# Optimization experiments

Hardware: AMD Instinct MI355X
Metric: run time of the kernel (lower is better)

The kernel has to match this reference:

```python
import jax, jax.numpy as jnp
import numpy as np

B, H, T, OUT, MLP_H = 4096, 1024, 60, 2, 64
IN = H + 4

def setup_inputs() -> dict:
    key = jax.random.key(0)
    ks = jax.random.split(key, 12)
    s = 1.0 / np.sqrt(H)
    return {
        "z": jax.random.normal(ks[0], (B, H), jnp.float32),
        "last_vel": jax.random.normal(ks[1], (B, 2), jnp.float32),
        "last_pos": jax.random.normal(ks[2], (B, 2), jnp.float32),
        "W_ih": jax.random.uniform(ks[3], (4 * H, IN), jnp.float32, -s, s),
        "W_hh": jax.random.uniform(ks[4], (4 * H, H), jnp.float32, -s, s),
        "b_ih": jax.random.uniform(ks[5], (4 * H,), jnp.float32, -s, s),
        "b_hh": jax.random.uniform(ks[6], (4 * H,), jnp.float32, -s, s),
        "W1": jax.random.uniform(ks[7], (MLP_H, H), jnp.float32, -s, s),
        "b1": jax.random.uniform(ks[8], (MLP_H,), jnp.float32, -s, s),
        "W2": jax.random.uniform(ks[9], (OUT, MLP_H), jnp.float32, -s, s),
        "b2": jax.random.uniform(ks[10], (OUT,), jnp.float32, -s, s),
    }

def _forward(z, last_vel, last_pos, W_ih, W_hh, b_ih, b_hh, W1, b1, W2, b2):
    z_aug = jnp.concatenate([z, last_pos, last_vel], axis=-1)  # (B, H+4)
    # input is identical at every timestep -> precompute input projection once
    x_gates = z_aug @ W_ih.T + b_ih + b_hh  # (B, 4H)

    def step(carry, _):
        h, c = carry
        gates = x_gates + h @ W_hh.T  # (B, 4H)
        i, f, g, o = jnp.split(gates, 4, axis=-1)  # torch gate order i,f,g,o
        i = jax.nn.sigmoid(i)
        f = jax.nn.sigmoid(f)
        g = jnp.tanh(g)
        o = jax.nn.sigmoid(o)
        c = f * c + i * g
        h = o * jnp.tanh(c)
        return (h, c), h

    h0 = jnp.zeros((z.shape[0], W_hh.shape[1]), z.dtype)
    _, hs = jax.lax.scan(step, (h0, h0), None, length=T)  # (T, B, H)
    out = jnp.transpose(hs, (1, 0, 2))  # (B, T, H)
    delta = jax.nn.relu(out @ W1.T + b1) @ W2.T + b2  # (B, T, 2)
    return jnp.cumsum(delta, axis=1) + last_pos[:, None, :]

def reference(z, last_vel, last_pos, W_ih, W_hh, b_ih, b_hh, W1, b1, W2, b2):
    return _forward(z, last_vel, last_pos, W_ih, W_hh, b_ih, b_hh, W1, b1, W2, b2)
```

## Files before the change

kernel.cpp:

```cpp
#include <hip/hip_runtime.h>
#include <stdint.h>

#define B_    4096
#define H_    1024
#define T_    60
#define IN_   1028
#define KA_   1056
#define G4_   4096
#define MLPH_ 64
#define NB_   6

typedef __attribute__((ext_vector_type(8))) short bf16x8;
typedef __attribute__((ext_vector_type(4))) float f32x4;
typedef __attribute__((ext_vector_type(4))) unsigned short u16x4;

#define GLOBAL_AS __attribute__((address_space(1)))
#define LDS_AS    __attribute__((address_space(3)))

__device__ __forceinline__ void gload_lds16(const void* g, void* l) {
  __builtin_amdgcn_global_load_lds((GLOBAL_AS void*)const_cast<void*>(g),
                                   (LDS_AS void*)l, 16, 0, 0);
}

__device__ __forceinline__ unsigned short f2bf(float f) {
  union { float f; unsigned int u; } v; v.f = f;
  unsigned int r = v.u + 0x7FFFu + ((v.u >> 16) & 1u);
  return (unsigned short)(r >> 16);
}

__device__ __forceinline__ float bf2f(unsigned short u) {
  union { unsigned int u; float f; } v; v.u = ((unsigned int)u) << 16;
  return v.f;
}

__device__ __forceinline__ float sigmf(float x) {
  float e = __expf(-x);
  return __builtin_amdgcn_rcpf(1.0f + e);
}

__device__ __forceinline__ float tanh_fast(float x) {
  x = fminf(fmaxf(x, -15.0f), 15.0f);
  float e = __expf(2.0f * x);
  return (e - 1.0f) * __builtin_amdgcn_rcpf(e + 1.0f);
}


__global__ void k_conv_bf16(const float* __restrict__ src,
                            unsigned short* __restrict__ dst, int n) {
  int i = blockIdx.x * blockDim.x + threadIdx.x;
  int stride = gridDim.x * blockDim.x;
  for (; i < n; i += stride) dst[i] = f2bf(src[i]);
}

__global__ void k_conv_wih(const float* __restrict__ w,
                           unsigned short* __restrict__ dst) {
  int i = blockIdx.x * blockDim.x + threadIdx.x;
  int stride = gridDim.x * blockDim.x;
  const int n = G4_ * KA_;
  for (; i < n; i += stride) {
    int r = i / KA_, k = i - r * KA_;
    dst[i] = (k < IN_) ? f2bf(w[(size_t)r * IN_ + k]) : (unsigned short)0;
  }
}

__global__ void k_build_zaug(const float* __restrict__ z,
                             const float* __restrict__ lp,
                             const float* __restrict__ lv,
                             unsigned short* __restrict__ dst) {
  int i = blockIdx.x * blockDim.x + threadIdx.x;
  int stride = gridDim.x * blockDim.x;
  const int n = B_ * KA_;
  for (; i < n; i += stride) {
    int b = i / KA_, k = i - b * KA_;
    float v;
    if (k < H_)            v = z[(size_t)b * H_ + k];
    else if (k < H_ + 2)   v = lp[b * 2 + (k - H_)];
    else if (k < IN_)      v = lv[b * 2 + (k - H_ - 2)];
    else                   v = 0.0f;
    dst[i] = f2bf(v);
  }
}


__global__ __launch_bounds__(256, 3) void k_xgates(
    const unsigned short* __restrict__ zaug, const unsigned short* __restrict__ wih,
    const float* __restrict__ bih, const float* __restrict__ bhh,
    u16x4* __restrict__ xg4) {
  __shared__ unsigned short As[128 * 32];
  __shared__ unsigned short Bs[128 * 32];
  const int tid = threadIdx.x, lane = tid & 63, wave = tid >> 6;
  const int bx = blockIdx.x, by = blockIdx.y;
  const int r_sub = lane >> 2;
  const int c16 = (lane & 3) * 16;

  f32x4 acc[2][8];
#pragma unroll
  for (int m = 0; m < 2; ++m)
#pragma unroll
    for (int n = 0; n < 8; ++n) acc[m][n] = {0.f, 0.f, 0.f, 0.f};

  for (int kk = 0; kk < KA_ / 32; ++kk) {
    const int k0 = kk * 32;
    __syncthreads();
#pragma unroll
    for (int i = 0; i < 2; ++i) {
      int ch = wave * 2 + i;
      int row = bx * 128 + ch * 16 + r_sub;
      gload_lds16((const char*)zaug + ((size_t)row * KA_ + k0) * 2 + c16,
                  (char*)As + ch * 1024);
    }
#pragma unroll
    for (int i = 0; i < 2; ++i) {
      int ch = wave * 2 + i;
      int g = ch >> 1;
      int wrow = g * H_ + by * 32 + (ch & 1) * 16 + r_sub;
      gload_lds16((const char*)wih + ((size_t)wrow * KA_ + k0) * 2 + c16,
                  (char*)Bs + ch * 1024);
    }
    __syncthreads();
    bf16x8 a[2], b[8];
#pragma unroll
    for (int m = 0; m < 2; ++m)
      a[m] = *(const bf16x8*)&As[(wave * 32 + m * 16 + (lane & 15)) * 32 + (lane >> 4) * 8];
#pragma unroll
    for (int n = 0; n < 8; ++n)
      b[n] = *(const bf16x8*)&Bs[(n * 16 + (lane & 15)) * 32 + (lane >> 4) * 8];
#pragma unroll
    for (int m = 0; m < 2; ++m)
#pragma unroll
      for (int n = 0; n < 8; ++n)
        acc[m][n] = __builtin_amdgcn_mfma_f32_16x16x32_bf16(a[m], b[n], acc[m][n], 0, 0, 0);
  }

  const int r0 = (lane >> 4) * 4, cl = lane & 15;
#pragma unroll
  for (int m = 0; m < 2; ++m)
#pragma unroll
    for (int j = 0; j < 4; ++j) {
      int row = bx * 128 + wave * 32 + m * 16 + r0 + j;
#pragma unroll
      for (int p = 0; p < 2; ++p) {
        int hc = by * 32 + p * 16 + cl;
        float iv = acc[m][0 + p][j] + bih[hc]        + bhh[hc];
        float fv = acc[m][2 + p][j] + bih[1024 + hc] + bhh[1024 + hc];
        float gv = acc[m][4 + p][j] + bih[2048 + hc] + bhh[2048 + hc];
        float ov = acc[m][6 + p][j] + bih[3072 + hc] + bhh[3072 + hc];
        u16x4 st = {f2bf(iv), f2bf(fv), f2bf(gv), f2bf(ov)};
        xg4[(size_t)row * H_ + hc] = st;
      }
    }
}


__global__ __launch_bounds__(256, 3) void k_step(
    const unsigned short* __restrict__ hprev, const unsigned short* __restrict__ whh,
    const u16x4* __restrict__ xg4, float* __restrict__ cbuf,
    unsigned short* __restrict__ hout) {
  __shared__ unsigned short As[128 * 32];
  __shared__ unsigned short Bs[128 * 32];
  const int tid = threadIdx.x, lane = tid & 63, wave = tid >> 6;
  const int bx = blockIdx.x, by = blockIdx.y;
  const int r_sub = lane >> 2;
  const int c16 = (lane & 3) * 16;

  f32x4 acc[2][8];
#pragma unroll
  for (int m = 0; m < 2; ++m)
#pragma unroll
    for (int n = 0; n < 8; ++n) acc[m][n] = {0.f, 0.f, 0.f, 0.f};

  for (int kk = 0; kk < H_ / 32; ++kk) {
    const int k0 = kk * 32;
    __syncthreads();
#pragma unroll
    for (int i = 0; i < 2; ++i) {
      int ch = wave * 2 + i;
      int row = bx * 128 + ch * 16 + r_sub;
      gload_lds16((const char*)hprev + ((size_t)row * H_ + k0) * 2 + c16,
                  (char*)As + ch * 1024);
    }
#pragma unroll
    for (int i = 0; i < 2; ++i) {
      int ch = wave * 2 + i;
      int g = ch >> 1;
      int wrow = g * H_ + by * 32 + (ch & 1) * 16 + r_sub;
      gload_lds16((const char*)whh + ((size_t)wrow * H_ + k0) * 2 + c16,
                  (char*)Bs + ch * 1024);
    }
    __syncthreads();
    bf16x8 a[2], b[8];
#pragma unroll
    for (int m = 0; m < 2; ++m)
      a[m] = *(const bf16x8*)&As[(wave * 32 + m * 16 + (lane & 15)) * 32 + (lane >> 4) * 8];
#pragma unroll
    for (int n = 0; n < 8; ++n)
      b[n] = *(const bf16x8*)&Bs[(n * 16 + (lane & 15)) * 32 + (lane >> 4) * 8];
#pragma unroll
    for (int m = 0; m < 2; ++m)
#pragma unroll
      for (int n = 0; n < 8; ++n)
        acc[m][n] = __builtin_amdgcn_mfma_f32_16x16x32_bf16(a[m], b[n], acc[m][n], 0, 0, 0);
  }

  const int r0 = (lane >> 4) * 4, cl = lane & 15;
#pragma unroll
  for (int m = 0; m < 2; ++m)
#pragma unroll
    for (int j = 0; j < 4; ++j) {
      int row = bx * 128 + wave * 32 + m * 16 + r0 + j;
#pragma unroll
      for (int p = 0; p < 2; ++p) {
        int hc = by * 32 + p * 16 + cl;
        u16x4 xv = xg4[(size_t)row * H_ + hc];
        float iv = sigmf(acc[m][0 + p][j] + bf2f(xv[0]));
        float fv = sigmf(acc[m][2 + p][j] + bf2f(xv[1]));
        float gv = tanh_fast(acc[m][4 + p][j] + bf2f(xv[2]));
        float ov = sigmf(acc[m][6 + p][j] + bf2f(xv[3]));
        size_t ci = (size_t)row * H_ + hc;
        float cv = fv * cbuf[ci] + iv * gv;
        cbuf[ci] = cv;
        hout[ci] = f2bf(ov * tanh_fast(cv));
      }
    }
}


__global__ __launch_bounds__(256) void k_mlp(
    const unsigned short* __restrict__ hring, const unsigned short* __restrict__ w1,
    const float* __restrict__ b1, const float* __restrict__ w2,
    const float* __restrict__ b2, float* __restrict__ delta, int t0) {
  __shared__ unsigned short As[64 * 32];
  __shared__ unsigned short Bs[64 * 32];
  __shared__ float hid[64][65];
  const int tid = threadIdx.x, lane = tid & 63, wave = tid >> 6;
  const int bx = blockIdx.x;
  const unsigned short* h = hring + (size_t)blockIdx.y * B_ * H_;
  const int t = t0 + blockIdx.y;
  const int r_sub = lane >> 2;
  const int c16 = (lane & 3) * 16;

  f32x4 acc[4];
#pragma unroll
  for (int n = 0; n < 4; ++n) acc[n] = {0.f, 0.f, 0.f, 0.f};

  for (int kk = 0; kk < H_ / 32; ++kk) {
    const int k0 = kk * 32;
    __syncthreads();
    {
      int row = bx * 64 + wave * 16 + r_sub;
      gload_lds16((const char*)h + ((size_t)row * H_ + k0) * 2 + c16,
                  (char*)As + wave * 1024);
    }
    {
      int jj = wave * 16 + r_sub;
      gload_lds16((const char*)w1 + ((size_t)jj * H_ + k0) * 2 + c16,
                  (char*)Bs + wave * 1024);
    }
    __syncthreads();
    bf16x8 a = *(const bf16x8*)&As[(wave * 16 + (lane & 15)) * 32 + (lane >> 4) * 8];
#pragma unroll
    for (int n = 0; n < 4; ++n) {
      bf16x8 b = *(const bf16x8*)&Bs[(n * 16 + (lane & 15)) * 32 + (lane >> 4) * 8];
      acc[n] = __builtin_amdgcn_mfma_f32_16x16x32_bf16(a, b, acc[n], 0, 0, 0);
    }
  }

  const int r0 = (lane >> 4) * 4, cl = lane & 15;
#pragma unroll
  for (int n = 0; n < 4; ++n)
#pragma unroll
    for (int j = 0; j < 4; ++j) {
      int row = wave * 16 + r0 + j;
      int col = n * 16 + cl;
      hid[row][col] = fmaxf(acc[n][j] + b1[col], 0.0f);
    }
  __syncthreads();

  if (tid < 128) {
    int r = tid >> 1, d = tid & 1;
    float s = b2[d];
#pragma unroll 8
    for (int k2 = 0; k2 < 64; ++k2) s += hid[r][k2] * w2[d * 64 + k2];
    delta[((size_t)(bx * 64 + r) * T_ + t) * 2 + d] = s;
  }
}


__global__ void k_cumsum(const float* __restrict__ delta,
                         const float* __restrict__ lp, float* __restrict__ out) {
  int id = blockIdx.x * blockDim.x + threadIdx.x;
  if (id >= B_ * 2) return;
  int b = id >> 1, d = id & 1;
  float cum = lp[b * 2 + d];
  size_t base = (size_t)b * T_ * 2 + d;
  for (int t = 0; t < T_; ++t) {
    cum += delta[base + t * 2];
    out[base + t * 2] = cum;
  }
}


extern "C" void kernel_launch(void* const* d_in, const int* in_sizes, int n_in,
                              void* d_out, int out_size, void* d_ws, size_t ws_size,
                              hipStream_t stream) {
  const float* z   = (const float*)d_in[0];
  const float* lv  = (const float*)d_in[1];
  const float* lp  = (const float*)d_in[2];
  const float* Wih = (const float*)d_in[3];
  const float* Whh = (const float*)d_in[4];
  const float* bih = (const float*)d_in[5];
  const float* bhh = (const float*)d_in[6];
  const float* W1  = (const float*)d_in[7];
  const float* b1  = (const float*)d_in[8];
  const float* W2  = (const float*)d_in[9];
  const float* b2  = (const float*)d_in[10];
  float* out = (float*)d_out;

  char* ws = (char*)d_ws;
  size_t off = 0;
  u16x4*          xg4    = (u16x4*)(ws + off);          off += (size_t)B_ * H_ * 8;
  unsigned short* whh_bf = (unsigned short*)(ws + off); off += (size_t)G4_ * H_ * 2;
  unsigned short* wih_bf = (unsigned short*)(ws + off); off += (size_t)G4_ * KA_ * 2;
  unsigned short* zaug   = (unsigned short*)(ws + off); off += (size_t)B_ * KA_ * 2;
  unsigned short* w1_bf  = (unsigned short*)(ws + off); off += (size_t)MLPH_ * H_ * 2;
  unsigned short* hring  = (unsigned short*)(ws + off); off += (size_t)NB_ * B_ * H_ * 2;
  float*          cbuf   = (float*)(ws + off);          off += (size_t)B_ * H_ * 4;
  float*          delta  = (float*)(ws + off);          off += (size_t)B_ * T_ * 2 * 4;

  const size_t BH = (size_t)B_ * H_;

  hipMemsetAsync(hring + (NB_ - 1) * BH, 0, BH * 2, stream);
  hipMemsetAsync(cbuf, 0, BH * 4, stream);

  k_conv_bf16 <<<2048, 256, 0, stream>>>(Whh, whh_bf, G4_ * H_);
  k_conv_wih  <<<2048, 256, 0, stream>>>(Wih, wih_bf);
  k_build_zaug<<<2048, 256, 0, stream>>>(z, lp, lv, zaug);
  k_conv_bf16 <<<256, 256, 0, stream>>>(W1, w1_bf, MLPH_ * H_);

  k_xgates<<<dim3(32, 32), 256, 0, stream>>>(zaug, wih_bf, bih, bhh, xg4);

  for (int t = 0; t < T_; ++t) {
    const unsigned short* hp = hring + (size_t)((t + NB_ - 1) % NB_) * BH;
    unsigned short*       hc = hring + (size_t)(t % NB_) * BH;
    k_step<<<dim3(32, 32), 256, 0, stream>>>(hp, whh_bf, xg4, cbuf, hc);
    if ((t % NB_) == NB_ - 1)
      k_mlp<<<dim3(64, NB_), 256, 0, stream>>>(hring, w1_bf, b1, W2, b2, delta, t - (NB_ - 1));
  }

  k_cumsum<<<32, 256, 0, stream>>>(delta, lp, out);
}
```

Before: 3.540 ms.

## Double-buffer LDS tiles and use 2x2 wave layout in LSTM GEMM kernels

Both the input-projection and recurrent-step GEMM kernels now double-buffer their LDS tiles. The next K-slice is prefetched with global_load_lds while MFMAs run on the current one, which removes one barrier per iteration. Waves are rearranged into a 2x2 grid, each computing 64 rows by 16 columns across all four gates, so fewer B fragments are read from LDS per MFMA and the bias loads are hoisted out of the epilogue loop. The occupancy hint rises to 4 blocks per CU, but the doubled LDS footprint and the larger accumulator set may limit occupancy.

```diff
diff --git a/kernel.cpp b/kernel.cpp
--- a/kernel.cpp
+++ b/kernel.cpp
@@ -82,145 +82,150 @@
 }
 
 
-__global__ __launch_bounds__(256, 3) void k_xgates(
+__global__ __launch_bounds__(256, 4) void k_xgates(
     const unsigned short* __restrict__ zaug, const unsigned short* __restrict__ wih,
     const float* __restrict__ bih, const float* __restrict__ bhh,
     u16x4* __restrict__ xg4) {
-  __shared__ unsigned short As[128 * 32];
-  __shared__ unsigned short Bs[128 * 32];
+  __shared__ unsigned short As[2][128 * 32];
+  __shared__ unsigned short Bs[2][128 * 32];
   const int tid = threadIdx.x, lane = tid & 63, wave = tid >> 6;
   const int bx = blockIdx.x, by = blockIdx.y;
-  const int r_sub = lane >> 2;
+  const int wm = wave >> 1, wn = wave & 1;
+  const int rs = lane >> 2;
   const int c16 = (lane & 3) * 16;
 
-  f32x4 acc[2][8];
-#pragma unroll
-  for (int m = 0; m < 2; ++m)
-#pragma unroll
-    for (int n = 0; n < 8; ++n) acc[m][n] = {0.f, 0.f, 0.f, 0.f};
-
-  for (int kk = 0; kk < KA_ / 32; ++kk) {
-    const int k0 = kk * 32;
+  const char* asrc0 = (const char*)zaug + ((size_t)(bx * 128 + (wave * 2 + 0) * 16 + rs) * KA_) * 2 + c16;
+  const char* asrc1 = (const char*)zaug + ((size_t)(bx * 128 + (wave * 2 + 1) * 16 + rs) * KA_) * 2 + c16;
+  const char* bsrc0 = (const char*)wih  + ((size_t)(wave * H_ + by * 32 +  0 + rs) * KA_) * 2 + c16;
+  const char* bsrc1 = (const char*)wih  + ((size_t)(wave * H_ + by * 32 + 16 + rs) * KA_) * 2 + c16;
+
+  f32x4 acc[4][4];
+#pragma unroll
+  for (int g = 0; g < 4; ++g)
+#pragma unroll
+    for (int m = 0; m < 4; ++m) acc[g][m] = {0.f, 0.f, 0.f, 0.f};
+
+  gload_lds16(asrc0, &As[0][(wave * 2 + 0) * 512]);
+  gload_lds16(asrc1, &As[0][(wave * 2 + 1) * 512]);
+  gload_lds16(bsrc0, &Bs[0][(wave * 2 + 0) * 512]);
+  gload_lds16(bsrc1, &Bs[0][(wave * 2 + 1) * 512]);
+  __syncthreads();
+
+  const int nt = KA_ / 32;
+  int cur = 0;
+  for (int kk = 0; kk < nt; ++kk) {
+    if (kk + 1 < nt) {
+      const size_t kb = (size_t)(kk + 1) * 64;
+      gload_lds16(asrc0 + kb, &As[cur ^ 1][(wave * 2 + 0) * 512]);
+      gload_lds16(asrc1 + kb, &As[cur ^ 1][(wave * 2 + 1) * 512]);
+      gload_lds16(bsrc0 + kb, &Bs[cur ^ 1][(wave * 2 + 0) * 512]);
+      gload_lds16(bsrc1 + kb, &Bs[cur ^ 1][(wave * 2 + 1) * 512]);
+    }
+    bf16x8 a[4], b[4];
+#pragma unroll
+    for (int m = 0; m < 4; ++m)
+      a[m] = *(const bf16x8*)&As[cur][(wm * 64 + m * 16 + (lane & 15)) * 32 + (lane >> 4) * 8];
+#pragma unroll
+    for (int g = 0; g < 4; ++g)
+      b[g] = *(const bf16x8*)&Bs[cur][((g * 2 + wn) * 16 + (lane & 15)) * 32 + (lane >> 4) * 8];
+#pragma unroll
+    for (int g = 0; g < 4; ++g)
+#pragma unroll
+      for (int m = 0; m < 4; ++m)
+        acc[g][m] = __builtin_amdgcn_mfma_f32_16x16x32_bf16(a[m], b[g], acc[g][m], 0, 0, 0);
     __syncthreads();
-#pragma unroll
-    for (int i = 0; i < 2; ++i) {
-      int ch = wave * 2 + i;
-      int row = bx * 128 + ch * 16 + r_sub;
-      gload_lds16((const char*)zaug + ((size_t)row * KA_ + k0) * 2 + c16,
-                  (char*)As + ch * 1024);
-    }
-#pragma unroll
-    for (int i = 0; i < 2; ++i) {
-      int ch = wave * 2 + i;
-      int g = ch >> 1;
-      int wrow = g * H_ + by * 32 + (ch & 1) * 16 + r_sub;
-      gload_lds16((const char*)wih + ((size_t)wrow * KA_ + k0) * 2 + c16,
-                  (char*)Bs + ch * 1024);
-    }
-    __syncthreads();
-    bf16x8 a[2], b[8];
-#pragma unroll
-    for (int m = 0; m < 2; ++m)
-      a[m] = *(const bf16x8*)&As[(wave * 32 + m * 16 + (lane & 15)) * 32 + (lane >> 4) * 8];
-#pragma unroll
-    for (int n = 0; n < 8; ++n)
-      b[n] = *(const bf16x8*)&Bs[(n * 16 + (lane & 15)) * 32 + (lane >> 4) * 8];
-#pragma unroll
-    for (int m = 0; m < 2; ++m)
-#pragma unroll
-      for (int n = 0; n < 8; ++n)
-        acc[m][n] = __builtin_amdgcn_mfma_f32_16x16x32_bf16(a[m], b[n], acc[m][n], 0, 0, 0);
+    cur ^= 1;
   }
 
   const int r0 = (lane >> 4) * 4, cl = lane & 15;
-#pragma unroll
-  for (int m = 0; m < 2; ++m)
+  const int hc = by * 32 + wn * 16 + cl;
+  const float bi = bih[hc]        + bhh[hc];
+  const float bf = bih[1024 + hc] + bhh[1024 + hc];
+  const float bg = bih[2048 + hc] + bhh[2048 + hc];
+  const float bo = bih[3072 + hc] + bhh[3072 + hc];
+#pragma unroll
+  for (int m = 0; m < 4; ++m)
 #pragma unroll
     for (int j = 0; j < 4; ++j) {
-      int row = bx * 128 + wave * 32 + m * 16 + r0 + j;
-#pragma unroll
-      for (int p = 0; p < 2; ++p) {
-        int hc = by * 32 + p * 16 + cl;
-        float iv = acc[m][0 + p][j] + bih[hc]        + bhh[hc];
-        float fv = acc[m][2 + p][j] + bih[1024 + hc] + bhh[1024 + hc];
-        float gv = acc[m][4 + p][j] + bih[2048 + hc] + bhh[2048 + hc];
-        float ov = acc[m][6 + p][j] + bih[3072 + hc] + bhh[3072 + hc];
-        u16x4 st = {f2bf(iv), f2bf(fv), f2bf(gv), f2bf(ov)};
-        xg4[(size_t)row * H_ + hc] = st;
-      }
-    }
-}
-
-
-__global__ __launch_bounds__(256, 3) void k_step(
+      int row = bx * 128 + wm * 64 + m * 16 + r0 + j;
+      u16x4 st = {f2bf(acc[0][m][j] + bi), f2bf(acc[1][m][j] + bf),
+                  f2bf(acc[2][m][j] + bg), f2bf(acc[3][m][j] + bo)};
+      xg4[(size_t)row * H_ + hc] = st;
+    }
+}
+
+
+__global__ __launch_bounds__(256, 4) void k_step(
     const unsigned short* __restrict__ hprev, const unsigned short* __restrict__ whh,
     const u16x4* __restrict__ xg4, float* __restrict__ cbuf,
     unsigned short* __restrict__ hout) {
-  __shared__ unsigned short As[128 * 32];
-  __shared__ unsigned short Bs[128 * 32];
+  __shared__ unsigned short As[2][128 * 32];
+  __shared__ unsigned short Bs[2][128 * 32];
   const int tid = threadIdx.x, lane = tid & 63, wave = tid >> 6;
   const int bx = blockIdx.x, by = blockIdx.y;
-  const int r_sub = lane >> 2;
+  const int wm = wave >> 1, wn = wave & 1;
+  const int rs = lane >> 2;
   const int c16 = (lane & 3) * 16;
 
-  f32x4 acc[2][8];
-#pragma unroll
-  for (int m = 0; m < 2; ++m)
-#pragma unroll
-    for (int n = 0; n < 8; ++n) acc[m][n] = {0.f, 0.f, 0.f, 0.f};
-
-  for (int kk = 0; kk < H_ / 32; ++kk) {
-    const int k0 = kk * 32;
+  const char* asrc0 = (const char*)hprev + ((size_t)(bx * 128 + (wave * 2 + 0) * 16 + rs) * H_) * 2 + c16;
+  const char* asrc1 = (const char*)hprev + ((size_t)(bx * 128 + (wave * 2 + 1) * 16 + rs) * H_) * 2 + c16;
+  const char* bsrc0 = (const char*)whh   + ((size_t)(wave * H_ + by * 32 +  0 + rs) * H_) * 2 + c16;
+  const char* bsrc1 = (const char*)whh   + ((size_t)(wave * H_ + by * 32 + 16 + rs) * H_) * 2 + c16;
+
+  f32x4 acc[4][4];
+#pragma unroll
+  for (int g = 0; g < 4; ++g)
+#pragma unroll
+    for (int m = 0; m < 4; ++m) acc[g][m] = {0.f, 0.f, 0.f, 0.f};
+
+  gload_lds16(asrc0, &As[0][(wave * 2 + 0) * 512]);
+  gload_lds16(asrc1, &As[0][(wave * 2 + 1) * 512]);
+  gload_lds16(bsrc0, &Bs[0][(wave * 2 + 0) * 512]);
+  gload_lds16(bsrc1, &Bs[0][(wave * 2 + 1) * 512]);
+  __syncthreads();
+
+  const int nt = H_ / 32;
+  int cur = 0;
+  for (int kk = 0; kk < nt; ++kk) {
+    if (kk + 1 < nt) {
+      const size_t kb = (size_t)(kk + 1) * 64;
+      gload_lds16(asrc0 + kb, &As[cur ^ 1][(wave * 2 + 0) * 512]);
+      gload_lds16(asrc1 + kb, &As[cur ^ 1][(wave * 2 + 1) * 512]);
+      gload_lds16(bsrc0 + kb, &Bs[cur ^ 1][(wave * 2 + 0) * 512]);
+      gload_lds16(bsrc1 + kb, &Bs[cur ^ 1][(wave * 2 + 1) * 512]);
+    }
+    bf16x8 a[4], b[4];
+#pragma unroll
+    for (int m = 0; m < 4; ++m)
+      a[m] = *(const bf16x8*)&As[cur][(wm * 64 + m * 16 + (lane & 15)) * 32 + (lane >> 4) * 8];
+#pragma unroll
+    for (int g = 0; g < 4; ++g)
+      b[g] = *(const bf16x8*)&Bs[cur][((g * 2 + wn) * 16 + (lane & 15)) * 32 + (lane >> 4) * 8];
+#pragma unroll
+    for (int g = 0; g < 4; ++g)
+#pragma unroll
+      for (int m = 0; m < 4; ++m)
+        acc[g][m] = __builtin_amdgcn_mfma_f32_16x16x32_bf16(a[m], b[g], acc[g][m], 0, 0, 0);
     __syncthreads();
-#pragma unroll
-    for (int i = 0; i < 2; ++i) {
-      int ch = wave * 2 + i;
-      int row = bx * 128 + ch * 16 + r_sub;
-      gload_lds16((const char*)hprev + ((size_t)row * H_ + k0) * 2 + c16,
-                  (char*)As + ch * 1024);
-    }
-#pragma unroll
-    for (int i = 0; i < 2; ++i) {
-      int ch = wave * 2 + i;
-      int g = ch >> 1;
-      int wrow = g * H_ + by * 32 + (ch & 1) * 16 + r_sub;
-      gload_lds16((const char*)whh + ((size_t)wrow * H_ + k0) * 2 + c16,
-                  (char*)Bs + ch * 1024);
-    }
-    __syncthreads();
-    bf16x8 a[2], b[8];
-#pragma unroll
-    for (int m = 0; m < 2; ++m)
-      a[m] = *(const bf16x8*)&As[(wave * 32 + m * 16 + (lane & 15)) * 32 + (lane >> 4) * 8];
-#pragma unroll
-    for (int n = 0; n < 8; ++n)
-      b[n] = *(const bf16x8*)&Bs[(n * 16 + (lane & 15)) * 32 + (lane >> 4) * 8];
-#pragma unroll
-    for (int m = 0; m < 2; ++m)
-#pragma unroll
-      for (int n = 0; n < 8; ++n)
-        acc[m][n] = __builtin_amdgcn_mfma_f32_16x16x32_bf16(a[m], b[n], acc[m][n], 0, 0, 0);
+    cur ^= 1;
   }
 
   const int r0 = (lane >> 4) * 4, cl = lane & 15;
-#pragma unroll
-  for (int m = 0; m < 2; ++m)
+  const int hc = by * 32 + wn * 16 + cl;
+#pragma unroll
+  for (int m = 0; m < 4; ++m)
 #pragma unroll
     for (int j = 0; j < 4; ++j) {
-      int row = bx * 128 + wave * 32 + m * 16 + r0 + j;
-#pragma unroll
-      for (int p = 0; p < 2; ++p) {
-        int hc = by * 32 + p * 16 + cl;
-        u16x4 xv = xg4[(size_t)row * H_ + hc];
-        float iv = sigmf(acc[m][0 + p][j] + bf2f(xv[0]));
-        float fv = sigmf(acc[m][2 + p][j] + bf2f(xv[1]));
-        float gv = tanh_fast(acc[m][4 + p][j] + bf2f(xv[2]));
-        float ov = sigmf(acc[m][6 + p][j] + bf2f(xv[3]));
-        size_t ci = (size_t)row * H_ + hc;
-        float cv = fv * cbuf[ci] + iv * gv;
-        cbuf[ci] = cv;
-        hout[ci] = f2bf(ov * tanh_fast(cv));
-      }
+      int row = bx * 128 + wm * 64 + m * 16 + r0 + j;
+      size_t ci = (size_t)row * H_ + hc;
+      u16x4 xv = xg4[ci];
+      float iv = sigmf(acc[0][m][j] + bf2f(xv[0]));
+      float fv = sigmf(acc[1][m][j] + bf2f(xv[1]));
+      float gv = tanh_fast(acc[2][m][j] + bf2f(xv[2]));
+      float ov = sigmf(acc[3][m][j] + bf2f(xv[3]));
+      float cv = fv * cbuf[ci] + iv * gv;
+      cbuf[ci] = cv;
+      hout[ci] = f2bf(ov * tanh_fast(cv));
     }
 }
 
```

Measured after the change: 2.974 ms. 16.0% less time.
